# Kernel tuning notes

Hardware: AMD Instinct MI355X
Metric: run time of the kernel (lower is better)

The kernel has to match this reference:

```python
import jax, jax.numpy as jnp
import numpy as np

EPS_LN = 1e-5

def layer_norm(x, g, b):
    mu = x.mean(-1, keepdims=True)
    var = ((x - mu) ** 2).mean(-1, keepdims=True)
    return (x - mu) / jnp.sqrt(var + EPS_LN) * g + b

def spike(x):
    # MultiSpike: quantized spike activation, forward = clip(round(x), 0, 4)
    return jnp.clip(jnp.round(x), 0.0, 4.0)

def setup_inputs() -> dict:
    key = jax.random.key(0)
    ks = jax.random.split(key, 8)
    B, C, H, W = 16, 256, 56, 56
    hid = 128
    inp = {}
    inp['feature_map'] = jax.random.normal(ks[0], (B, C, H, W), jnp.float32)
    inp['audio_feature'] = jax.random.normal(ks[1], (B, 1, C), jnp.float32)
    # MINE params
    inp['w1'] = jax.random.normal(ks[2], (hid, 2 * C), jnp.float32) / np.sqrt(2 * C)
    inp['b1'] = jnp.zeros((hid,), jnp.float32)
    inp['g1'] = jnp.ones((hid,), jnp.float32)
    inp['beta1'] = jnp.zeros((hid,), jnp.float32)
    inp['w2'] = jax.random.normal(ks[3], (hid // 2, hid), jnp.float32) / np.sqrt(hid)
    inp['b2'] = jnp.zeros((hid // 2,), jnp.float32)
    inp['g2'] = jnp.ones((hid // 2,), jnp.float32)
    inp['beta2'] = jnp.zeros((hid // 2,), jnp.float32)
    inp['w3'] = jax.random.normal(ks[4], (1, hid // 2), jnp.float32) / np.sqrt(hid // 2)
    inp['b3'] = jnp.zeros((1,), jnp.float32)
    # MI params
    inp['pw'] = jax.random.normal(ks[5], (C, C), jnp.float32) / np.sqrt(C)
    inp['pb'] = jnp.zeros((C,), jnp.float32)
    inp['pg'] = jnp.ones((C,), jnp.float32)
    inp['pbeta'] = jnp.zeros((C,), jnp.float32)
    return inp

def reference(feature_map, audio_feature, w1, b1, g1, beta1, w2, b2, g2, beta2,
              w3, b3, pw, pb, pg, pbeta):
    B, C, H, W = feature_map.shape
    # visual tokens: [B*H*W, C]
    visual = feature_map.transpose(0, 2, 3, 1).reshape(B * H * W, C)
    # broadcast audio to every spatial position: [B*H*W, C]
    audio = jnp.broadcast_to(audio_feature[:, 0][:, None, None, :], (B, H, W, C)).reshape(B * H * W, C)
    # MINE MLP on joint features
    joint = jnp.concatenate([visual, audio], axis=1)            # [BHW, 2C]
    h = spike(layer_norm(joint @ w1.T + b1, g1, beta1))          # [BHW, 128]
    h = spike(layer_norm(h @ w2.T + b2, g2, beta2))              # [BHW, 64]
    mi = (h @ w3.T + b3)[:, 0]                                   # [BHW]
    mi_map = mi.reshape(B, 1, H * W)
    fm_flat = feature_map.reshape(B, C, H * W)
    # MI-weighted pooling: [B,1,C]
    x = jnp.einsum('bos,bcs->boc', mi_map, fm_flat)
    x = x @ pw.T + pb                                            # proj (dropout = eval identity)
    x = spike(layer_norm(x, pg, pbeta))                          # [B,1,C]
    fusion_map = jnp.einsum('bchw,bc->bchw', feature_map, x[:, 0])
    mi4 = mi_map.reshape(B, 1, H, W)
    mi4 = (mi4 - mi4.min()) / (mi4.max() - mi4.min() + 1e-6)     # global min-max norm
    return fusion_map, mi4
```

## Files before the change

kernel.cpp:

```cpp
#include <hip/hip_runtime.h>

#define HW 3136
#define NPOS 12845056

__device__ __forceinline__ unsigned fkey(float f) {
  unsigned u = __float_as_uint(f);
  return (u & 0x80000000u) ? ~u : (u | 0x80000000u);
}
__device__ __forceinline__ float funkey(unsigned u) {
  return __uint_as_float((u & 0x80000000u) ? (u & 0x7FFFFFFFu) : ~u);
}
__device__ __forceinline__ float spikef(float x) {
  return fminf(fmaxf(rintf(x), 0.0f), 4.0f);
}

__global__ __launch_bounds__(256) void prep_kernel(
    const float* __restrict__ audio, const float* __restrict__ w1,
    const float* __restrict__ b1, const float* __restrict__ w2,
    float* __restrict__ a_pre, float* __restrict__ w1t,
    float* __restrict__ w2t, float* __restrict__ pool,
    unsigned* __restrict__ mm)
{
  __shared__ float au[256];
  const int bx = blockIdx.x, t = threadIdx.x;
  if (bx < 128) {
    int idx = bx * 256 + t;
    int c = idx >> 7, j = idx & 127;
    w1t[idx] = w1[j * 512 + c];
  } else if (bx < 160) {
    int idx = (bx - 128) * 256 + t;
    int k = idx >> 6, j2 = idx & 63;
    w2t[idx] = w2[j2 * 128 + k];
  } else if (bx < 176) {
    int b = bx - 160;
    au[t] = audio[b * 256 + t];
    __syncthreads();
    int w = t >> 6, l = t & 63;
    float a0 = au[l], a1 = au[l + 64], a2 = au[l + 128], a3 = au[l + 192];
    for (int jj = 0; jj < 32; ++jj) {
      int j = w * 32 + jj;
      const float* row = w1 + j * 512 + 256;
      float s = row[l] * a0 + row[l + 64] * a1 + row[l + 128] * a2 + row[l + 192] * a3;
      #pragma unroll
      for (int off = 32; off; off >>= 1) s += __shfl_xor(s, off);
      if (l == 0) a_pre[b * 128 + j] = s + b1[j];
    }
  } else {
    for (int i = t; i < 4096; i += 256) pool[i] = 0.0f;
    if (t == 0) { mm[0] = 0xFFFFFFFFu; mm[1] = 0u; }
  }
}

__global__ __launch_bounds__(256, 3) void mlp_kernel(
    const float* __restrict__ fm, const float* __restrict__ w1t,
    const float* __restrict__ w2t, const float* __restrict__ b2,
    const float* __restrict__ w3, const float* __restrict__ b3,
    const float* __restrict__ g1, const float* __restrict__ be1,
    const float* __restrict__ g2, const float* __restrict__ be2,
    const float* __restrict__ a_pre, float* __restrict__ mi_out,
    float* __restrict__ pool, unsigned* __restrict__ mm)
{
  __shared__ float h1f[128 * 64];
  __shared__ float red[8][64];

  const int b  = blockIdx.y;
  const int s0 = blockIdx.x * 64;
  const int t  = threadIdx.x;
  const int l  = t & 63;
  const int wv = __builtin_amdgcn_readfirstlane(t >> 6);

  const float* fmblk = fm + (size_t)b * 256 * HW + s0;

  float acc[32];
  #pragma unroll
  for (int j = 0; j < 32; ++j) acc[j] = 0.f;
  {
    const float*  fp = fmblk + l;
    const float4* wr = (const float4*)(w1t + wv * 32);
    #pragma unroll 4
    for (int k = 0; k < 256; ++k) {
      float x = *fp; fp += HW;
      #pragma unroll
      for (int q = 0; q < 8; ++q) {
        float4 w4 = wr[q];
        acc[4*q+0] = fmaf(x, w4.x, acc[4*q+0]);
        acc[4*q+1] = fmaf(x, w4.y, acc[4*q+1]);
        acc[4*q+2] = fmaf(x, w4.z, acc[4*q+2]);
        acc[4*q+3] = fmaf(x, w4.w, acc[4*q+3]);
      }
      wr += 32;
    }
  }
  {
    const float4* ap = (const float4*)(a_pre + b * 128 + wv * 32);
    #pragma unroll
    for (int q = 0; q < 8; ++q) {
      float4 a4 = ap[q];
      acc[4*q+0] += a4.x; acc[4*q+1] += a4.y;
      acc[4*q+2] += a4.z; acc[4*q+3] += a4.w;
    }
  }

  float mu, inv;
  {
    float s = 0.f;
    #pragma unroll
    for (int j = 0; j < 32; ++j) s += acc[j];
    red[wv][l] = s;
    __syncthreads();
    mu = (red[0][l] + red[1][l] + red[2][l] + red[3][l]) * (1.0f/128.0f);
    float s2 = 0.f;
    #pragma unroll
    for (int j = 0; j < 32; ++j) { float d = acc[j] - mu; s2 = fmaf(d, d, s2); }
    red[4 + wv][l] = s2;
    __syncthreads();
    float var = (red[4][l] + red[5][l] + red[6][l] + red[7][l]) * (1.0f/128.0f);
    inv = 1.0f / sqrtf(var + 1e-5f);
  }

  {
    const float* gp = g1  + wv * 32;
    const float* bp = be1 + wv * 32;
    #pragma unroll
    for (int j = 0; j < 32; ++j) {
      float h = spikef((acc[j] - mu) * inv * gp[j] + bp[j]);
      h1f[(wv * 32 + j) * 64 + l] = h;
    }
  }
  __syncthreads();

  float a2[16];
  #pragma unroll
  for (int j = 0; j < 16; ++j) a2[j] = 0.f;
  {
    const float*  hp = h1f + l;
    const float4* wr = (const float4*)(w2t + wv * 16);
    #pragma unroll 4
    for (int k = 0; k < 128; ++k) {
      float h = *hp; hp += 64;
      #pragma unroll
      for (int q = 0; q < 4; ++q) {
        float4 w4 = wr[q];
        a2[4*q+0] = fmaf(h, w4.x, a2[4*q+0]);
        a2[4*q+1] = fmaf(h, w4.y, a2[4*q+1]);
        a2[4*q+2] = fmaf(h, w4.z, a2[4*q+2]);
        a2[4*q+3] = fmaf(h, w4.w, a2[4*q+3]);
      }
      wr += 16;
    }
  }
  {
    const float4* bp = (const float4*)(b2 + wv * 16);
    #pragma unroll
    for (int q = 0; q < 4; ++q) {
      float4 b4 = bp[q];
      a2[4*q+0] += b4.x; a2[4*q+1] += b4.y;
      a2[4*q+2] += b4.z; a2[4*q+3] += b4.w;
    }
  }

  float mu2, inv2;
  {
    float s = 0.f;
    #pragma unroll
    for (int j = 0; j < 16; ++j) s += a2[j];
    red[wv][l] = s;
    __syncthreads();
    mu2 = (red[0][l] + red[1][l] + red[2][l] + red[3][l]) * (1.0f/64.0f);
    float s2 = 0.f;
    #pragma unroll
    for (int j = 0; j < 16; ++j) { float d = a2[j] - mu2; s2 = fmaf(d, d, s2); }
    red[4 + wv][l] = s2;
    __syncthreads();
    float var = (red[4][l] + red[5][l] + red[6][l] + red[7][l]) * (1.0f/64.0f);
    inv2 = 1.0f / sqrtf(var + 1e-5f);
  }

  {
    const float* gp = g2  + wv * 16;
    const float* bp = be2 + wv * 16;
    const float* wp = w3  + wv * 16;
    float p = 0.f;
    #pragma unroll
    for (int j = 0; j < 16; ++j) {
      float sp = spikef((a2[j] - mu2) * inv2 * gp[j] + bp[j]);
      p = fmaf(sp, wp[j], p);
    }
    red[wv][l] = p;
  }
  __syncthreads();
  const float mi = red[0][l] + red[1][l] + red[2][l] + red[3][l] + b3[0];

  if (wv == 0) {
    mi_out[b * HW + s0 + l] = mi;
    float mn = mi, mx = mi;
    #pragma unroll
    for (int off = 32; off; off >>= 1) {
      mn = fminf(mn, __shfl_xor(mn, off));
      mx = fmaxf(mx, __shfl_xor(mx, off));
    }
    if (l == 0) {
      unsigned kmn = fkey(mn), kmx = fkey(mx);
      volatile unsigned* vmm = (volatile unsigned*)mm;
      if (kmn < vmm[0]) atomicMin(&mm[0], kmn);
      if (kmx > vmm[1]) atomicMax(&mm[1], kmx);
    }
  }

  {
    const float* fp = fmblk + l + (size_t)(wv << 6) * HW;
    #pragma unroll 4
    for (int ci = 0; ci < 64; ++ci) {
      float v = *fp * mi; fp += HW;
      #pragma unroll
      for (int off = 32; off; off >>= 1) v += __shfl_xor(v, off);
      if (l == 0) atomicAdd(&pool[b * 256 + (wv << 6) + ci], v);
    }
  }
}

__global__ __launch_bounds__(256) void scale_kernel(
    const float* __restrict__ pool, const float* __restrict__ pw,
    const float* __restrict__ pb, const float* __restrict__ pg,
    const float* __restrict__ pbeta, float* __restrict__ scale,
    const unsigned* __restrict__ mm, float* __restrict__ gpar)
{
  __shared__ float pl[256];
  __shared__ float xsh[256];
  __shared__ float rs[4], rs2[4];
  int b = blockIdx.x, t = threadIdx.x;
  pl[t] = pool[b*256 + t];
  __syncthreads();
  int w = t >> 6, l = t & 63;
  float p0 = pl[l], p1 = pl[l+64], p2 = pl[l+128], p3 = pl[l+192];
  for (int jj = 0; jj < 64; ++jj) {
    int j = w*64 + jj;
    const float* row = pw + j*256;
    float s = row[l]*p0 + row[l+64]*p1 + row[l+128]*p2 + row[l+192]*p3;
    #pragma unroll
    for (int off = 32; off; off >>= 1) s += __shfl_xor(s, off);
    if (l == 0) xsh[j] = s;
  }
  __syncthreads();
  float x = xsh[t] + pb[t];
  float s = x;
  #pragma unroll
  for (int off = 32; off; off >>= 1) s += __shfl_xor(s, off);
  if (l == 0) rs[w] = s;
  __syncthreads();
  float mu = (rs[0]+rs[1]+rs[2]+rs[3]) * (1.0f/256.0f);
  float d = x - mu;
  float s2 = d*d;
  #pragma unroll
  for (int off = 32; off; off >>= 1) s2 += __shfl_xor(s2, off);
  if (l == 0) rs2[w] = s2;
  __syncthreads();
  float var = (rs2[0]+rs2[1]+rs2[2]+rs2[3]) * (1.0f/256.0f);
  float v = d / sqrtf(var + 1e-5f) * pg[t] + pbeta[t];
  scale[b*256 + t] = spikef(v);
  if (b == 0 && t == 0) {
    float mn = funkey(mm[0]), mx = funkey(mm[1]);
    gpar[0] = mn;
    gpar[1] = mx - mn + 1e-6f;
  }
}

__global__ __launch_bounds__(256) void fuse_kernel(
    const float4* __restrict__ fm4, const float* __restrict__ scale,
    const float4* __restrict__ mi4, const float* __restrict__ gpar,
    float4* __restrict__ out4, float4* __restrict__ mi4out)
{
  const int c = blockIdx.x, b = blockIdx.y, t = threadIdx.x;
  if (c < 256) {
    float s = scale[b * 256 + c];
    size_t base = ((size_t)b * 256 + c) * 784;
    #pragma unroll
    for (int i = 0; i < 3; ++i) {
      int idx = t + i * 256;
      float4 v = fm4[base + idx];
      out4[base + idx] = make_float4(v.x*s, v.y*s, v.z*s, v.w*s);
    }
    int idx = t + 768;
    if (idx < 784) {
      float4 v = fm4[base + idx];
      out4[base + idx] = make_float4(v.x*s, v.y*s, v.z*s, v.w*s);
    }
  } else {
    float gmin = gpar[0], den = gpar[1];
    size_t base = (size_t)b * 784;
    #pragma unroll
    for (int i = 0; i < 3; ++i) {
      int idx = t + i * 256;
      float4 v = mi4[base + idx];
      mi4out[base + idx] = make_float4((v.x-gmin)/den, (v.y-gmin)/den,
                                       (v.z-gmin)/den, (v.w-gmin)/den);
    }
    int idx = t + 768;
    if (idx < 784) {
      float4 v = mi4[base + idx];
      mi4out[base + idx] = make_float4((v.x-gmin)/den, (v.y-gmin)/den,
                                       (v.z-gmin)/den, (v.w-gmin)/den);
    }
  }
}

extern "C" void kernel_launch(void* const* d_in, const int* in_sizes, int n_in,
                              void* d_out, int out_size, void* d_ws, size_t ws_size,
                              hipStream_t stream)
{
  const float* fm    = (const float*)d_in[0];
  const float* audio = (const float*)d_in[1];
  const float* w1    = (const float*)d_in[2];
  const float* b1    = (const float*)d_in[3];
  const float* g1    = (const float*)d_in[4];
  const float* be1   = (const float*)d_in[5];
  const float* w2    = (const float*)d_in[6];
  const float* b2    = (const float*)d_in[7];
  const float* g2    = (const float*)d_in[8];
  const float* be2   = (const float*)d_in[9];
  const float* w3    = (const float*)d_in[10];
  const float* b3    = (const float*)d_in[11];
  const float* pw    = (const float*)d_in[12];
  const float* pb    = (const float*)d_in[13];
  const float* pg    = (const float*)d_in[14];
  const float* pbeta = (const float*)d_in[15];

  float* ws    = (float*)d_ws;
  float* a_pre = ws;
  float* pool  = ws + 2048;
  float* scale = ws + 6144;
  float* mi    = ws + 10240;
  float* w1t   = ws + 60416;
  float* w2t   = ws + 93184;
  unsigned* mm = (unsigned*)(ws + 101376);
  float* gpar  = ws + 101378;

  float* out    = (float*)d_out;
  float* mi4out = out + NPOS;

  prep_kernel<<<177, 256, 0, stream>>>(audio, w1, b1, w2, a_pre, w1t, w2t,
                                       pool, mm);
  mlp_kernel<<<dim3(49, 16), 256, 0, stream>>>(fm, w1t, w2t, b2, w3, b3,
                                               g1, be1, g2, be2,
                                               a_pre, mi, pool, mm);
  scale_kernel<<<16, 256, 0, stream>>>(pool, pw, pb, pg, pbeta, scale, mm, gpar);
  fuse_kernel<<<dim3(257, 16), 256, 0, stream>>>((const float4*)fm, scale,
                                                 (const float4*)mi, gpar,
                                                 (float4*)out, (float4*)mi4out);
}
```

Measured before the change: 287.0 us.

## Register-tile the MINE MLP GEMMs with double-buffered LDS staging via global_load_lds

Rewrites mlp_kernel to use 128 threads, each computing an 8x8 register tile (8 positions x 8 hidden units). The feature-map and w1t chunks are staged into double-buffered shared memory with direct global-to-LDS loads, so the next chunk loads while the current one is computed. Layer-norm reductions now use shuffles plus a two-wave shared-memory exchange. The goal is more FMA work per load, replacing the old pattern of one scalar load per k per thread. The cost is more registers, fewer waves per block, and a pooling loop where each wave now handles 128 channels.

New measurement: 414.7 us. 44.5% more time.

```diff
diff --git a/kernel.cpp b/kernel.cpp
--- a/kernel.cpp
+++ b/kernel.cpp
@@ -51,7 +51,7 @@
   }
 }
 
-__global__ __launch_bounds__(256, 3) void mlp_kernel(
+__global__ __launch_bounds__(128) void mlp_kernel(
     const float* __restrict__ fm, const float* __restrict__ w1t,
     const float* __restrict__ w2t, const float* __restrict__ b2,
     const float* __restrict__ w3, const float* __restrict__ b3,
@@ -60,161 +60,281 @@
     const float* __restrict__ a_pre, float* __restrict__ mi_out,
     float* __restrict__ pool, unsigned* __restrict__ mm)
 {
-  __shared__ float h1f[128 * 64];
-  __shared__ float red[8][64];
+  __shared__ __align__(16) float smem[12288];
+  __shared__ __align__(16) float red[2][2][64];
+  __shared__ float miL[64];
 
   const int b  = blockIdx.y;
   const int s0 = blockIdx.x * 64;
   const int t  = threadIdx.x;
   const int l  = t & 63;
-  const int wv = __builtin_amdgcn_readfirstlane(t >> 6);
+  const int w  = __builtin_amdgcn_readfirstlane(t >> 6);
+  const int pg = l & 7;
+  const int jg = l >> 3;
 
   const float* fmblk = fm + (size_t)b * 256 * HW + s0;
 
-  float acc[32];
+  auto stage = [&](int ch, int bd) {
+    #pragma unroll
+    for (int i = 0; i < 4; ++i) {
+      const float* g = fmblk + (size_t)(ch * 32 + (w * 4 + i) * 4 + (l >> 4)) * HW
+                       + (l & 15) * 4;
+      float* d = smem + bd * 2048 + (w * 4 + i) * 256;
+      __builtin_amdgcn_global_load_lds(
+          (const __attribute__((address_space(1))) void*)g,
+          (__attribute__((address_space(3))) void*)d, 16, 0, 0);
+    }
+    #pragma unroll
+    for (int i = 0; i < 8; ++i) {
+      const float* g = w1t + (size_t)(ch * 32 + (w * 8 + i) * 2 + (l >> 5)) * 128
+                       + (l & 31) * 4;
+      float* d = smem + 4096 + bd * 4096 + (w * 8 + i) * 256;
+      __builtin_amdgcn_global_load_lds(
+          (const __attribute__((address_space(1))) void*)g,
+          (__attribute__((address_space(3))) void*)d, 16, 0, 0);
+    }
+  };
+
+  float acc[8][8];
   #pragma unroll
-  for (int j = 0; j < 32; ++j) acc[j] = 0.f;
-  {
-    const float*  fp = fmblk + l;
-    const float4* wr = (const float4*)(w1t + wv * 32);
+  for (int ii = 0; ii < 8; ++ii)
+    #pragma unroll
+    for (int jj = 0; jj < 8; ++jj) acc[ii][jj] = 0.f;
+
+  stage(0, 0);
+  __syncthreads();
+  #pragma unroll 1
+  for (int ch = 0; ch < 8; ++ch) {
+    if (ch < 7) stage(ch + 1, (ch + 1) & 1);
+    const float* Ab = smem + (ch & 1) * 2048;
+    const float* Bb = smem + 4096 + (ch & 1) * 4096;
     #pragma unroll 4
-    for (int k = 0; k < 256; ++k) {
-      float x = *fp; fp += HW;
-      #pragma unroll
-      for (int q = 0; q < 8; ++q) {
-        float4 w4 = wr[q];
-        acc[4*q+0] = fmaf(x, w4.x, acc[4*q+0]);
-        acc[4*q+1] = fmaf(x, w4.y, acc[4*q+1]);
-        acc[4*q+2] = fmaf(x, w4.z, acc[4*q+2]);
-        acc[4*q+3] = fmaf(x, w4.w, acc[4*q+3]);
+    for (int k = 0; k < 32; ++k) {
+      float4 a0 = *(const float4*)(Ab + k * 64 + pg * 8);
+      float4 a1 = *(const float4*)(Ab + k * 64 + pg * 8 + 4);
+      float4 b0 = *(const float4*)(Bb + k * 128 + w * 64 + jg * 8);
+      float4 b1 = *(const float4*)(Bb + k * 128 + w * 64 + jg * 8 + 4);
+      float av[8] = {a0.x, a0.y, a0.z, a0.w, a1.x, a1.y, a1.z, a1.w};
+      float bv[8] = {b0.x, b0.y, b0.z, b0.w, b1.x, b1.y, b1.z, b1.w};
+      #pragma unroll
+      for (int ii = 0; ii < 8; ++ii)
+        #pragma unroll
+        for (int jj = 0; jj < 8; ++jj)
+          acc[ii][jj] = fmaf(av[ii], bv[jj], acc[ii][jj]);
+    }
+    __syncthreads();
+  }
+  {
+    const float* ap = a_pre + b * 128 + w * 64 + jg * 8;
+    float4 a40 = *(const float4*)(ap);
+    float4 a41 = *(const float4*)(ap + 4);
+    float av[8] = {a40.x, a40.y, a40.z, a40.w, a41.x, a41.y, a41.z, a41.w};
+    #pragma unroll
+    for (int ii = 0; ii < 8; ++ii)
+      #pragma unroll
+      for (int jj = 0; jj < 8; ++jj) acc[ii][jj] += av[jj];
+  }
+
+  float mu[8], inv[8];
+  {
+    float s[8];
+    #pragma unroll
+    for (int ii = 0; ii < 8; ++ii) {
+      float v = 0.f;
+      #pragma unroll
+      for (int jj = 0; jj < 8; ++jj) v += acc[ii][jj];
+      v += __shfl_xor(v, 8); v += __shfl_xor(v, 16); v += __shfl_xor(v, 32);
+      s[ii] = v;
+    }
+    if (jg == 0) {
+      *(float4*)&red[0][w][pg * 8]     = make_float4(s[0], s[1], s[2], s[3]);
+      *(float4*)&red[0][w][pg * 8 + 4] = make_float4(s[4], s[5], s[6], s[7]);
+    }
+    __syncthreads();
+    float4 rA0 = *(const float4*)&red[0][0][pg * 8];
+    float4 rA1 = *(const float4*)&red[0][0][pg * 8 + 4];
+    float4 rB0 = *(const float4*)&red[0][1][pg * 8];
+    float4 rB1 = *(const float4*)&red[0][1][pg * 8 + 4];
+    mu[0] = (rA0.x + rB0.x) * (1.0f/128.0f); mu[1] = (rA0.y + rB0.y) * (1.0f/128.0f);
+    mu[2] = (rA0.z + rB0.z) * (1.0f/128.0f); mu[3] = (rA0.w + rB0.w) * (1.0f/128.0f);
+    mu[4] = (rA1.x + rB1.x) * (1.0f/128.0f); mu[5] = (rA1.y + rB1.y) * (1.0f/128.0f);
+    mu[6] = (rA1.z + rB1.z) * (1.0f/128.0f); mu[7] = (rA1.w + rB1.w) * (1.0f/128.0f);
+    #pragma unroll
+    for (int ii = 0; ii < 8; ++ii) {
+      float v = 0.f;
+      #pragma unroll
+      for (int jj = 0; jj < 8; ++jj) { float d = acc[ii][jj] - mu[ii]; v = fmaf(d, d, v); }
+      v += __shfl_xor(v, 8); v += __shfl_xor(v, 16); v += __shfl_xor(v, 32);
+      s[ii] = v;
+    }
+    if (jg == 0) {
+      *(float4*)&red[1][w][pg * 8]     = make_float4(s[0], s[1], s[2], s[3]);
+      *(float4*)&red[1][w][pg * 8 + 4] = make_float4(s[4], s[5], s[6], s[7]);
+    }
+    __syncthreads();
+    float4 vA0 = *(const float4*)&red[1][0][pg * 8];
+    float4 vA1 = *(const float4*)&red[1][0][pg * 8 + 4];
+    float4 vB0 = *(const float4*)&red[1][1][pg * 8];
+    float4 vB1 = *(const float4*)&red[1][1][pg * 8 + 4];
+    inv[0] = 1.0f / sqrtf((vA0.x + vB0.x) * (1.0f/128.0f) + 1e-5f);
+    inv[1] = 1.0f / sqrtf((vA0.y + vB0.y) * (1.0f/128.0f) + 1e-5f);
+    inv[2] = 1.0f / sqrtf((vA0.z + vB0.z) * (1.0f/128.0f) + 1e-5f);
+    inv[3] = 1.0f / sqrtf((vA0.w + vB0.w) * (1.0f/128.0f) + 1e-5f);
+    inv[4] = 1.0f / sqrtf((vA1.x + vB1.x) * (1.0f/128.0f) + 1e-5f);
+    inv[5] = 1.0f / sqrtf((vA1.y + vB1.y) * (1.0f/128.0f) + 1e-5f);
+    inv[6] = 1.0f / sqrtf((vA1.z + vB1.z) * (1.0f/128.0f) + 1e-5f);
+    inv[7] = 1.0f / sqrtf((vA1.w + vB1.w) * (1.0f/128.0f) + 1e-5f);
+  }
+
+  {
+    const float* gp = g1  + w * 64 + jg * 8;
+    const float* bp = be1 + w * 64 + jg * 8;
+    float4 g40 = *(const float4*)(gp), g41 = *(const float4*)(gp + 4);
+    float4 b40 = *(const float4*)(bp), b41 = *(const float4*)(bp + 4);
+    float gv[8] = {g40.x, g40.y, g40.z, g40.w, g41.x, g41.y, g41.z, g41.w};
+    float bv[8] = {b40.x, b40.y, b40.z, b40.w, b41.x, b41.y, b41.z, b41.w};
+    #pragma unroll
+    for (int jj = 0; jj < 8; ++jj) {
+      float4 h0, h1v;
+      h0.x = spikef((acc[0][jj] - mu[0]) * inv[0] * gv[jj] + bv[jj]);
+      h0.y = spikef((acc[1][jj] - mu[1]) * inv[1] * gv[jj] + bv[jj]);
+      h0.z = spikef((acc[2][jj] - mu[2]) * inv[2] * gv[jj] + bv[jj]);
+      h0.w = spikef((acc[3][jj] - mu[3]) * inv[3] * gv[jj] + bv[jj]);
+      h1v.x = spikef((acc[4][jj] - mu[4]) * inv[4] * gv[jj] + bv[jj]);
+      h1v.y = spikef((acc[5][jj] - mu[5]) * inv[5] * gv[jj] + bv[jj]);
+      h1v.z = spikef((acc[6][jj] - mu[6]) * inv[6] * gv[jj] + bv[jj]);
+      h1v.w = spikef((acc[7][jj] - mu[7]) * inv[7] * gv[jj] + bv[jj]);
+      float* hrow = smem + (w * 64 + jg * 8 + jj) * 64 + pg * 8;
+      *(float4*)(hrow) = h0;
+      *(float4*)(hrow + 4) = h1v;
+    }
+  }
+  __syncthreads();
+
+  float acc2[8][4];
+  #pragma unroll
+  for (int ii = 0; ii < 8; ++ii)
+    #pragma unroll
+    for (int jj = 0; jj < 4; ++jj) acc2[ii][jj] = 0.f;
+  {
+    const float* w2p = w2t + (w << 5) + (jg << 2);
+    #pragma unroll 4
+    for (int k2 = 0; k2 < 128; ++k2) {
+      float4 a0 = *(const float4*)(smem + k2 * 64 + pg * 8);
+      float4 a1 = *(const float4*)(smem + k2 * 64 + pg * 8 + 4);
+      float4 wv = *(const float4*)(w2p + (k2 << 6));
+      float av[8] = {a0.x, a0.y, a0.z, a0.w, a1.x, a1.y, a1.z, a1.w};
+      float bv[4] = {wv.x, wv.y, wv.z, wv.w};
+      #pragma unroll
+      for (int ii = 0; ii < 8; ++ii)
+        #pragma unroll
+        for (int jj = 0; jj < 4; ++jj)
+          acc2[ii][jj] = fmaf(av[ii], bv[jj], acc2[ii][jj]);
+    }
+  }
+  {
+    float4 b4 = *(const float4*)(b2 + (w << 5) + (jg << 2));
+    float bv[4] = {b4.x, b4.y, b4.z, b4.w};
+    #pragma unroll
+    for (int ii = 0; ii < 8; ++ii)
+      #pragma unroll
+      for (int jj = 0; jj < 4; ++jj) acc2[ii][jj] += bv[jj];
+  }
+
+  float mi[8];
+  {
+    float s[8], mu2[8], inv2[8];
+    #pragma unroll
+    for (int ii = 0; ii < 8; ++ii) {
+      float v = acc2[ii][0] + acc2[ii][1] + acc2[ii][2] + acc2[ii][3];
+      v += __shfl_xor(v, 8); v += __shfl_xor(v, 16); v += __shfl_xor(v, 32);
+      s[ii] = v;
+    }
+    if (jg == 0) {
+      *(float4*)&red[0][w][pg * 8]     = make_float4(s[0], s[1], s[2], s[3]);
+      *(float4*)&red[0][w][pg * 8 + 4] = make_float4(s[4], s[5], s[6], s[7]);
+    }
+    __syncthreads();
+    #pragma unroll
+    for (int ii = 0; ii < 8; ++ii)
+      mu2[ii] = (red[0][0][pg * 8 + ii] + red[0][1][pg * 8 + ii]) * (1.0f/64.0f);
+    #pragma unroll
+    for (int ii = 0; ii < 8; ++ii) {
+      float v = 0.f;
+      #pragma unroll
+      for (int jj = 0; jj < 4; ++jj) { float d = acc2[ii][jj] - mu2[ii]; v = fmaf(d, d, v); }
+      v += __shfl_xor(v, 8); v += __shfl_xor(v, 16); v += __shfl_xor(v, 32);
+      s[ii] = v;
+    }
+    if (jg == 0) {
+      *(float4*)&red[1][w][pg * 8]     = make_float4(s[0], s[1], s[2], s[3]);
+      *(float4*)&red[1][w][pg * 8 + 4] = make_float4(s[4], s[5], s[6], s[7]);
+    }
+    __syncthreads();
+    #pragma unroll
+    for (int ii = 0; ii < 8; ++ii)
+      inv2[ii] = 1.0f / sqrtf((red[1][0][pg * 8 + ii] + red[1][1][pg * 8 + ii])
+                              * (1.0f/64.0f) + 1e-5f);
+    float4 g4  = *(const float4*)(g2  + (w << 5) + (jg << 2));
+    float4 be4 = *(const float4*)(be2 + (w << 5) + (jg << 2));
+    float4 w34 = *(const float4*)(w3  + (w << 5) + (jg << 2));
+    float gv[4] = {g4.x, g4.y, g4.z, g4.w};
+    float bv[4] = {be4.x, be4.y, be4.z, be4.w};
+    float wv[4] = {w34.x, w34.y, w34.z, w34.w};
+    #pragma unroll
+    for (int ii = 0; ii < 8; ++ii) {
+      float p = 0.f;
+      #pragma unroll
+      for (int jj = 0; jj < 4; ++jj) {
+        float sp = spikef((acc2[ii][jj] - mu2[ii]) * inv2[ii] * gv[jj] + bv[jj]);
+        p = fmaf(sp, wv[jj], p);
       }
-      wr += 32;
-    }
-  }
-  {
-    const float4* ap = (const float4*)(a_pre + b * 128 + wv * 32);
-    #pragma unroll
-    for (int q = 0; q < 8; ++q) {
-      float4 a4 = ap[q];
-      acc[4*q+0] += a4.x; acc[4*q+1] += a4.y;
-      acc[4*q+2] += a4.z; acc[4*q+3] += a4.w;
-    }
-  }
-
-  float mu, inv;
-  {
-    float s = 0.f;
-    #pragma unroll
-    for (int j = 0; j < 32; ++j) s += acc[j];
-    red[wv][l] = s;
-    __syncthreads();
-    mu = (red[0][l] + red[1][l] + red[2][l] + red[3][l]) * (1.0f/128.0f);
-    float s2 = 0.f;
-    #pragma unroll
-    for (int j = 0; j < 32; ++j) { float d = acc[j] - mu; s2 = fmaf(d, d, s2); }
-    red[4 + wv][l] = s2;
-    __syncthreads();
-    float var = (red[4][l] + red[5][l] + red[6][l] + red[7][l]) * (1.0f/128.0f);
-    inv = 1.0f / sqrtf(var + 1e-5f);
-  }
-
-  {
-    const float* gp = g1  + wv * 32;
-    const float* bp = be1 + wv * 32;
-    #pragma unroll
-    for (int j = 0; j < 32; ++j) {
-      float h = spikef((acc[j] - mu) * inv * gp[j] + bp[j]);
-      h1f[(wv * 32 + j) * 64 + l] = h;
-    }
-  }
-  __syncthreads();
-
-  float a2[16];
-  #pragma unroll
-  for (int j = 0; j < 16; ++j) a2[j] = 0.f;
-  {
-    const float*  hp = h1f + l;
-    const float4* wr = (const float4*)(w2t + wv * 16);
-    #pragma unroll 4
-    for (int k = 0; k < 128; ++k) {
-      float h = *hp; hp += 64;
-      #pragma unroll
-      for (int q = 0; q < 4; ++q) {
-        float4 w4 = wr[q];
-        a2[4*q+0] = fmaf(h, w4.x, a2[4*q+0]);
-        a2[4*q+1] = fmaf(h, w4.y, a2[4*q+1]);
-        a2[4*q+2] = fmaf(h, w4.z, a2[4*q+2]);
-        a2[4*q+3] = fmaf(h, w4.w, a2[4*q+3]);
-      }
-      wr += 16;
-    }
-  }
-  {
-    const float4* bp = (const float4*)(b2 + wv * 16);
-    #pragma unroll
-    for (int q = 0; q < 4; ++q) {
-      float4 b4 = bp[q];
-      a2[4*q+0] += b4.x; a2[4*q+1] += b4.y;
-      a2[4*q+2] += b4.z; a2[4*q+3] += b4.w;
-    }
-  }
-
-  float mu2, inv2;
-  {
-    float s = 0.f;
-    #pragma unroll
-    for (int j = 0; j < 16; ++j) s += a2[j];
-    red[wv][l] = s;
-    __syncthreads();
-    mu2 = (red[0][l] + red[1][l] + red[2][l] + red[3][l]) * (1.0f/64.0f);
-    float s2 = 0.f;
-    #pragma unroll
-    for (int j = 0; j < 16; ++j) { float d = a2[j] - mu2; s2 = fmaf(d, d, s2); }
-    red[4 + wv][l] = s2;
-    __syncthreads();
-    float var = (red[4][l] + red[5][l] + red[6][l] + red[7][l]) * (1.0f/64.0f);
-    inv2 = 1.0f / sqrtf(var + 1e-5f);
-  }
-
-  {
-    const float* gp = g2  + wv * 16;
-    const float* bp = be2 + wv * 16;
-    const float* wp = w3  + wv * 16;
-    float p = 0.f;
-    #pragma unroll
-    for (int j = 0; j < 16; ++j) {
-      float sp = spikef((a2[j] - mu2) * inv2 * gp[j] + bp[j]);
-      p = fmaf(sp, wp[j], p);
-    }
-    red[wv][l] = p;
-  }
-  __syncthreads();
-  const float mi = red[0][l] + red[1][l] + red[2][l] + red[3][l] + b3[0];
-
-  if (wv == 0) {
-    mi_out[b * HW + s0 + l] = mi;
-    float mn = mi, mx = mi;
-    #pragma unroll
-    for (int off = 32; off; off >>= 1) {
-      mn = fminf(mn, __shfl_xor(mn, off));
-      mx = fmaxf(mx, __shfl_xor(mx, off));
-    }
-    if (l == 0) {
+      p += __shfl_xor(p, 8); p += __shfl_xor(p, 16); p += __shfl_xor(p, 32);
+      s[ii] = p;
+    }
+    if (jg == 0) {
+      *(float4*)&red[0][w][pg * 8]     = make_float4(s[0], s[1], s[2], s[3]);
+      *(float4*)&red[0][w][pg * 8 + 4] = make_float4(s[4], s[5], s[6], s[7]);
+    }
+    __syncthreads();
+    const float b3v = b3[0];
+    #pragma unroll
+    for (int ii = 0; ii < 8; ++ii)
+      mi[ii] = red[0][0][pg * 8 + ii] + red[0][1][pg * 8 + ii] + b3v;
+  }
+
+  if (w == 0 && jg == 0) {
+    float* mo = mi_out + b * HW + s0 + pg * 8;
+    *(float4*)(mo)     = make_float4(mi[0], mi[1], mi[2], mi[3]);
+    *(float4*)(mo + 4) = make_float4(mi[4], mi[5], mi[6], mi[7]);
+    *(float4*)&miL[pg * 8]     = make_float4(mi[0], mi[1], mi[2], mi[3]);
+    *(float4*)&miL[pg * 8 + 4] = make_float4(mi[4], mi[5], mi[6], mi[7]);
+  }
+  {
+    float mn = mi[0], mx = mi[0];
+    #pragma unroll
+    for (int ii = 1; ii < 8; ++ii) { mn = fminf(mn, mi[ii]); mx = fmaxf(mx, mi[ii]); }
+    mn = fminf(mn, __shfl_xor(mn, 1)); mx = fmaxf(mx, __shfl_xor(mx, 1));
+    mn = fminf(mn, __shfl_xor(mn, 2)); mx = fmaxf(mx, __shfl_xor(mx, 2));
+    mn = fminf(mn, __shfl_xor(mn, 4)); mx = fmaxf(mx, __shfl_xor(mx, 4));
+    if (t == 0) {
       unsigned kmn = fkey(mn), kmx = fkey(mx);
       volatile unsigned* vmm = (volatile unsigned*)mm;
       if (kmn < vmm[0]) atomicMin(&mm[0], kmn);
       if (kmx > vmm[1]) atomicMax(&mm[1], kmx);
     }
   }
-
-  {
-    const float* fp = fmblk + l + (size_t)(wv << 6) * HW;
+  __syncthreads();
+
+  {
+    const float ml = miL[l];
+    const float* fp2 = fmblk + l + (size_t)(w << 7) * HW;
     #pragma unroll 4
-    for (int ci = 0; ci < 64; ++ci) {
-      float v = *fp * mi; fp += HW;
+    for (int ci = 0; ci < 128; ++ci) {
+      float v = fp2[(size_t)ci * HW] * ml;
       #pragma unroll
       for (int off = 32; off; off >>= 1) v += __shfl_xor(v, off);
-      if (l == 0) atomicAdd(&pool[b * 256 + (wv << 6) + ci], v);
+      if (l == 0) atomicAdd(&pool[b * 256 + (w << 7) + ci], v);
     }
   }
 }
@@ -340,7 +460,7 @@
 
   prep_kernel<<<177, 256, 0, stream>>>(audio, w1, b1, w2, a_pre, w1t, w2t,
                                        pool, mm);
-  mlp_kernel<<<dim3(49, 16), 256, 0, stream>>>(fm, w1t, w2t, b2, w3, b3,
+  mlp_kernel<<<dim3(49, 16), 128, 0, stream>>>(fm, w1t, w2t, b2, w3, b3,
                                                g1, be1, g2, be2,
                                                a_pre, mi, pool, mm);
   scale_kernel<<<16, 256, 0, stream>>>(pool, pw, pb, pg, pbeta, scale, mm, gpar);
```
